# Optimization experiments

Measured on AMD Instinct MI355X. Metric: run time of the kernel, lower is better.

The kernel has to match this reference:

```python
import jax, jax.numpy as jnp
import numpy as np

LAMBDA = 0.5
ALPHA_PRE = 1.0
ALPHA_DA = 1.0

B, N, C, T, O = 8, 1024, 64, 12, 64


def setup_inputs() -> dict:
    key = jax.random.key(0)
    ks = jax.random.split(key, 10)
    s = 0.1  # keep tanh out of deep saturation, like xavier-init scales
    return {
        "x": jax.random.normal(ks[0], (B, N, C, T), dtype=jnp.float32),
        "static_adj": jax.random.uniform(ks[1], (N, N), dtype=jnp.float32) / N,
        "W0": jax.random.normal(ks[2], (C, O), dtype=jnp.float32) * s,
        "b0": jax.random.normal(ks[3], (O,), dtype=jnp.float32) * s,
        "Ws": jax.random.normal(ks[4], (T, C, O), dtype=jnp.float32) * s,
        "bs": jax.random.normal(ks[5], (T, O), dtype=jnp.float32) * s,
        "Wd": jax.random.normal(ks[6], (T, C, O), dtype=jnp.float32) * s,
        "bd": jax.random.normal(ks[7], (T, O), dtype=jnp.float32) * s,
        "E1": jax.random.normal(ks[8], (T, N, O), dtype=jnp.float32) * s,
        "E2": jax.random.normal(ks[9], (T, N, O), dtype=jnp.float32) * s,
    }


def reference(x, static_adj, W0, b0, Ws, bs, Wd, bd, E1, E2):
    # x: [B,N,C,T] -> [T,B,N,C] so the per-timestep layers vectorize over leading T.
    xt = jnp.transpose(x, (3, 0, 1, 2))  # [T,B,N,C]
    n = xt.shape[2]

    # shared top-level linear
    x0 = jnp.einsum('tbnc,co->tbno', xt, W0) + b0  # [T,B,N,O]

    # static GCN per timestep: linear(static_adj @ x_t)
    sagg = jnp.einsum('nm,tbmc->tbnc', static_adj, xt)
    static_out = jnp.einsum('tbnc,tco->tbno', sagg, Ws) + bs[:, None, None, :]

    # dynamic GCN: base = linear_t(x_t)
    base = jnp.einsum('tbnc,tco->tbno', xt, Wd) + bd[:, None, None, :]
    DE1 = jnp.tanh(ALPHA_PRE * (base * E1[:, None]))  # [T,B,N,O]
    DE2 = jnp.tanh(ALPHA_PRE * (base * E2[:, None]))
    # cross = DE1@DE2^T - DE2@DE1^T = M - M^T
    M = jnp.einsum('tbno,tbmo->tbnm', DE1, DE2)  # [T,B,N,N]
    DA = jax.nn.relu(jnp.tanh(ALPHA_DA * (M - jnp.swapaxes(M, -1, -2))))

    # symmetric degree normalization of (DA + I)
    DA = DA + jnp.eye(n, dtype=DA.dtype)
    rowsum = jnp.clip(DA.sum(axis=-1), 1e-12, None)
    d_inv_sqrt = rowsum ** -0.5
    DA = DA * d_inv_sqrt[..., :, None] * d_inv_sqrt[..., None, :]

    dagg = jnp.einsum('tbnm,tbmc->tbnc', DA, xt)
    dyn_out = jnp.einsum('tbnc,tco->tbno', dagg, Wd) + bd[:, None, None, :]

    fused = (LAMBDA - 0.025) * static_out + (1.0 - LAMBDA - 0.025) * dyn_out + 0.05 * x0
    return jnp.transpose(fused, (1, 2, 3, 0))  # [B,N,O,T]
```

## Files before the change

kernel.cpp:

```cpp
#include <hip/hip_runtime.h>

#define BB 8
#define NN 1024
#define CC 64
#define TT 12
#define OO 64

typedef unsigned short u16;
typedef __attribute__((ext_vector_type(8))) short s16x8;
typedef __attribute__((ext_vector_type(4))) float f32x4;
typedef __attribute__((ext_vector_type(4))) unsigned int u32x4;
typedef __attribute__((ext_vector_type(2))) unsigned int u32x2;

__device__ __forceinline__ u16 f2bu(float f){
  union { float f; unsigned u; } v; v.f = f;
  unsigned r = v.u + 0x7FFFu + ((v.u >> 16) & 1u);
  return (u16)(r >> 16);
}
__device__ __forceinline__ float b2f(u16 h){
  union { unsigned u; float f; } v; v.u = ((unsigned)h) << 16; return v.f;
}
__device__ __forceinline__ float relu_tanh(float d){
  float e = __expf(2.0f * d);
  return fmaxf(1.0f - 2.0f * __builtin_amdgcn_rcpf(e + 1.0f), 0.0f);
}
__device__ __forceinline__ float tanh_fast(float d){
  float e = __expf(2.0f * d);
  return 1.0f - 2.0f * __builtin_amdgcn_rcpf(e + 1.0f);
}
__device__ __forceinline__ float tanh_sgn(float x){
  float ax = fabsf(x);
  float e = __expf(2.0f * ax);
  float t = 1.0f - 2.0f * __builtin_amdgcn_rcpf(e + 1.0f);
  return x < 0.0f ? -t : t;
}

#define MFMA16(a,b,c) __builtin_amdgcn_mfma_f32_16x16x32_bf16((a),(b),(c),0,0,0)

__device__ __forceinline__ s16x8 ld72(const u16* s, int row0, int ko, int lane){
  return *(const s16x8*)(s + (row0 + (lane & 15)) * 72 + ko + ((lane >> 4) << 3));
}

__global__ __launch_bounds__(256) void k0_transpose(const float* __restrict__ x,
                                                    u16* __restrict__ xt){
  const int n = blockIdx.x, b = blockIdx.y;
  __shared__ float s[CC*TT];
  const float* src = x + (size_t)(b*NN + n)*CC*TT;
  for (int k = threadIdx.x; k < CC*TT; k += 256) s[k] = src[k];
  __syncthreads();
  for (int k = threadIdx.x; k < CC*TT; k += 256){
    const int t = k >> 6, c = k & 63;
    xt[(((size_t)t*BB + b)*NN + n)*CC + c] = f2bu(s[c*TT + t]);
  }
}

__global__ __launch_bounds__(256) void kprep(const float* __restrict__ adj,
                                             u16* __restrict__ adjb,
                                             float* __restrict__ rs){
  const size_t i = ((size_t)blockIdx.x*256 + threadIdx.x)*4;
  if (i < (size_t)NN*NN){
    const float4 v = *(const float4*)(adj + i);
    u16 o0=f2bu(v.x), o1=f2bu(v.y), o2=f2bu(v.z), o3=f2bu(v.w);
    adjb[i]=o0; adjb[i+1]=o1; adjb[i+2]=o2; adjb[i+3]=o3;
  }
  const size_t j = (size_t)blockIdx.x*256 + threadIdx.x;
  if (j < (size_t)TT*BB*NN) rs[j] = 1.0f;
}

__global__ __launch_bounds__(256) void k1_de(const u16* __restrict__ xt,
    const float* __restrict__ Wd, const float* __restrict__ bd,
    const float* __restrict__ E1, const float* __restrict__ E2,
    u16* __restrict__ DE1g, u16* __restrict__ DE2g){
  __shared__ __align__(16) u16 sWd[64*72];
  const int tid = threadIdx.x, lane = tid & 63, wid = tid >> 6;
  const int l15 = lane & 15, lr4 = lane >> 4;
  const int it = blockIdx.x, b = blockIdx.y, t = blockIdx.z;
  const int n0 = it * 64;
  for (int k = tid; k < 4096; k += 256){
    const int o = k & 63, c = k >> 6;
    sWd[o*72 + c] = f2bu(Wd[(size_t)t*4096 + c*64 + o]);
  }
  __syncthreads();
  const size_t tb = (size_t)t*BB + b;
  const u16* gx = xt + (tb*NN + n0)*CC;
  const int wrow = wid * 16;
  const f32x4 fz = {0.f,0.f,0.f,0.f};
  f32x4 acc[4] = {fz, fz, fz, fz};
  #pragma unroll
  for (int ks = 0; ks < 2; ++ks){
    const int ko = ks*32;
    const s16x8 a = *(const s16x8*)(gx + (wrow + l15)*CC + ko + (lr4 << 3));
    #pragma unroll
    for (int v = 0; v < 4; ++v)
      acc[v] = MFMA16(a, ld72(sWd, v*16, ko, lane), acc[v]);
  }
  #pragma unroll
  for (int v = 0; v < 4; ++v){
    const int o = v*16 + l15;
    const float bdv = bd[t*OO + o];
    #pragma unroll
    for (int e = 0; e < 4; ++e){
      const int n = n0 + wrow + (lr4 << 2) + e;
      const float base = acc[v][e] + bdv;
      const size_t eo = ((size_t)t*NN + n)*OO + o;
      const size_t so = (tb*NN + n)*OO + o;
      DE1g[so] = f2bu(tanh_sgn(base * E1[eo]));
      DE2g[so] = f2bu(tanh_sgn(base * E2[eo]));
    }
  }
}

__global__ __launch_bounds__(256) void k2a(const u16* __restrict__ DE1g,
    const u16* __restrict__ DE2g, float* __restrict__ rowsum){
  __shared__ __align__(16) u16 sb0[64*72], sb1[64*72];
  __shared__ __align__(16) u16 sb2[64*72], sb3[64*72];
  const int tid = threadIdx.x, lane = tid & 63, wid = tid >> 6;
  const int l15 = lane & 15, lr4 = lane >> 4;
  const int nwg = 8*BB*TT;
  const int logical = ((int)blockIdx.x & 7)*(nwg >> 3) + ((int)blockIdx.x >> 3);
  const int p = logical & 7;
  const size_t tb = (size_t)(logical >> 3);
  const int tiA = p, tiB = 15 - p;
  const u16* g1 = DE1g + tb*NN*OO;
  const u16* g2 = DE2g + tb*NN*OO;
  for (int k = tid; k < 512; k += 256){
    const int r = k >> 3, c = (k & 7) << 3;
    *(s16x8*)(sb0 + r*72 + c) = *(const s16x8*)(g1 + (size_t)(tiA*64 + r)*OO + c);
    s16x8 vA = *(const s16x8*)(g2 + (size_t)(tiA*64 + r)*OO + c);
    u32x4 wA = *(u32x4*)&vA; wA ^= 0x80008000u;
    *(u32x4*)(sb1 + r*72 + c) = wA;
    *(s16x8*)(sb2 + r*72 + c) = *(const s16x8*)(g1 + (size_t)(tiB*64 + r)*OO + c);
    s16x8 vB = *(const s16x8*)(g2 + (size_t)(tiB*64 + r)*OO + c);
    u32x4 wB = *(u32x4*)&vB; wB ^= 0x80008000u;
    *(u32x4*)(sb3 + r*72 + c) = wB;
  }
  __syncthreads();
  const int wrow = wid * 16;
  s16x8 a1A[2], na2A[2], a1B[2], na2B[2];
  #pragma unroll
  for (int ks = 0; ks < 2; ++ks){
    a1A[ks]  = ld72(sb0, wrow, ks*32, lane);
    na2A[ks] = ld72(sb1, wrow, ks*32, lane);
    a1B[ks]  = ld72(sb2, wrow, ks*32, lane);
    na2B[ks] = ld72(sb3, wrow, ks*32, lane);
  }
  const int srow = tid >> 2, sc0 = (tid & 3) << 4;
  s16x8 pB1a,pB1b, pB2a,pB2b;
#define LOADT(TJ) do { \
    pB1a = *(const s16x8*)(g2 + (size_t)((TJ)*64 + srow)*OO + sc0); \
    pB1b = *(const s16x8*)(g2 + (size_t)((TJ)*64 + srow)*OO + sc0 + 8); \
    pB2a = *(const s16x8*)(g1 + (size_t)((TJ)*64 + srow)*OO + sc0); \
    pB2b = *(const s16x8*)(g1 + (size_t)((TJ)*64 + srow)*OO + sc0 + 8); \
  } while (0)
  LOADT(p);
  float rpA[4] = {0.f,0.f,0.f,0.f}, rpB[4] = {0.f,0.f,0.f,0.f};
  const f32x4 fz = {0.f,0.f,0.f,0.f};
  float* rsg = rowsum + tb*NN;
  __syncthreads();
  for (int tj = p; tj < 16; ++tj){
    u16* sJ1 = ((tj - p) & 1) ? sb2 : sb0;
    u16* sJ2 = ((tj - p) & 1) ? sb3 : sb1;
    *(s16x8*)(sJ1 + srow*72 + sc0)     = pB1a;
    *(s16x8*)(sJ1 + srow*72 + sc0 + 8) = pB1b;
    *(s16x8*)(sJ2 + srow*72 + sc0)     = pB2a;
    *(s16x8*)(sJ2 + srow*72 + sc0 + 8) = pB2b;
    __syncthreads();
    if (tj < 15) LOADT(tj + 1);
    s16x8 b1[4], b2[4], b1h[4], b2h[4];
    #pragma unroll
    for (int v = 0; v < 4; ++v){
      b1[v]  = ld72(sJ1, v*16, 0,  lane);
      b2[v]  = ld72(sJ2, v*16, 0,  lane);
      b1h[v] = ld72(sJ1, v*16, 32, lane);
      b2h[v] = ld72(sJ2, v*16, 32, lane);
    }
    {
      f32x4 z[4];
      #pragma unroll
      for (int v = 0; v < 4; ++v){
        z[v] = MFMA16(a1A[0],  b1[v],  fz);
        z[v] = MFMA16(na2A[0], b2[v],  z[v]);
        z[v] = MFMA16(a1A[1],  b1h[v], z[v]);
        z[v] = MFMA16(na2A[1], b2h[v], z[v]);
      }
      float colp[4] = {0.f,0.f,0.f,0.f};
      #pragma unroll
      for (int v = 0; v < 4; ++v)
        #pragma unroll
        for (int e = 0; e < 4; ++e){
          const float th = tanh_fast(z[v][e]);
          rpA[e]  += fmaxf(th, 0.f);
          colp[v] += fmaxf(-th, 0.f);
        }
      if (tj > tiA){
        #pragma unroll
        for (int v = 0; v < 4; ++v){
          float c = colp[v];
          c += __shfl_xor(c, 16); c += __shfl_xor(c, 32);
          if (lane < 16) atomicAdd(&rsg[tj*64 + v*16 + lane], c);
        }
      }
    }
    if (tj >= tiB){
      f32x4 z[4];
      #pragma unroll
      for (int v = 0; v < 4; ++v){
        z[v] = MFMA16(a1B[0],  b1[v],  fz);
        z[v] = MFMA16(na2B[0], b2[v],  z[v]);
        z[v] = MFMA16(a1B[1],  b1h[v], z[v]);
        z[v] = MFMA16(na2B[1], b2h[v], z[v]);
      }
      float colp[4] = {0.f,0.f,0.f,0.f};
      #pragma unroll
      for (int v = 0; v < 4; ++v)
        #pragma unroll
        for (int e = 0; e < 4; ++e){
          const float th = tanh_fast(z[v][e]);
          rpB[e]  += fmaxf(th, 0.f);
          colp[v] += fmaxf(-th, 0.f);
        }
      if (tj > tiB){
        #pragma unroll
        for (int v = 0; v < 4; ++v){
          float c = colp[v];
          c += __shfl_xor(c, 16); c += __shfl_xor(c, 32);
          if (lane < 16) atomicAdd(&rsg[tj*64 + v*16 + lane], c);
        }
      }
    }
  }
#undef LOADT
  #pragma unroll
  for (int e = 0; e < 4; ++e){
    float r = rpA[e];
    r += __shfl_xor(r, 1); r += __shfl_xor(r, 2);
    r += __shfl_xor(r, 4); r += __shfl_xor(r, 8);
    if (l15 == 0) atomicAdd(&rsg[tiA*64 + wrow + (lr4 << 2) + e], r);
  }
  #pragma unroll
  for (int e = 0; e < 4; ++e){
    float r = rpB[e];
    r += __shfl_xor(r, 1); r += __shfl_xor(r, 2);
    r += __shfl_xor(r, 4); r += __shfl_xor(r, 8);
    if (l15 == 0) atomicAdd(&rsg[tiB*64 + wrow + (lr4 << 2) + e], r);
  }
}

__global__ __launch_bounds__(256) void k3b(const u16* __restrict__ xt,
    const float* __restrict__ Wd, const float* __restrict__ Ws,
    const float* __restrict__ W0, const float* __restrict__ bd,
    const float* __restrict__ bs, const float* __restrict__ b0,
    const float* __restrict__ rowsum, u16* __restrict__ xdvT,
    u16* __restrict__ xswT, u16* __restrict__ x0w){
  __shared__ __align__(16) u16 sW[64*72];
  const int tid = threadIdx.x, lane = tid & 63, wid = tid >> 6;
  const int l15 = lane & 15, lr4 = lane >> 4;
  const int it = blockIdx.x, b = blockIdx.y, t = blockIdx.z;
  const size_t tb = (size_t)t*BB + b;
  const int n0 = it * 128, wrow = wid * 32;
  const float* dvb = rowsum + tb*NN + n0;
  float dis[2][4];
  #pragma unroll
  for (int u = 0; u < 2; ++u)
    #pragma unroll
    for (int e = 0; e < 4; ++e)
      dis[u][e] = rsqrtf(dvb[wrow + u*16 + (lr4 << 2) + e]);
  float badd[4];
  #pragma unroll
  for (int v = 0; v < 4; ++v){
    const int o = v*16 + l15;
    badd[v] = 0.475f*(bd[t*OO + o] + bs[t*OO + o]) + 0.05f*b0[o];
  }
  const u16* gx = xt + (tb*NN + n0)*CC;
  const f32x4 fz = {0.f,0.f,0.f,0.f};
  for (int pass = 0; pass < 3; ++pass){
    __syncthreads();
    {
      const float* Wsrc = (pass == 0) ? (Wd + (size_t)t*4096)
                        : (pass == 1) ? (Ws + (size_t)t*4096) : W0;
      const float scale = (pass == 2) ? 0.05f : 0.475f;
      for (int k = tid; k < 4096; k += 256){
        const int o = k & 63, c = k >> 6;
        sW[o*72 + c] = f2bu(scale * Wsrc[c*64 + o]);
      }
    }
    __syncthreads();
    f32x4 acc[2][4];
    #pragma unroll
    for (int u = 0; u < 2; ++u)
      #pragma unroll
      for (int v = 0; v < 4; ++v) acc[u][v] = fz;
    #pragma unroll
    for (int ks = 0; ks < 2; ++ks){
      const int ko = ks*32;
      s16x8 bw[4];
      #pragma unroll
      for (int v = 0; v < 4; ++v) bw[v] = ld72(sW, v*16, ko, lane);
      #pragma unroll
      for (int u = 0; u < 2; ++u){
        const s16x8 a = *(const s16x8*)(gx + (wrow + u*16 + l15)*CC + ko + (lr4 << 3));
        #pragma unroll
        for (int v = 0; v < 4; ++v) acc[u][v] = MFMA16(a, bw[v], acc[u][v]);
      }
    }
    #pragma unroll
    for (int u = 0; u < 2; ++u)
      #pragma unroll
      for (int v = 0; v < 4; ++v){
        const int o = v*16 + l15;
        #pragma unroll
        for (int e = 0; e < 4; ++e){
          const int nl = wrow + u*16 + (lr4 << 2) + e;
          float val = acc[u][v][e];
          if (pass == 0)      xdvT[(tb*OO + o)*NN + n0 + nl] = f2bu(val * dis[u][e]);
          else if (pass == 1) xswT[(tb*OO + o)*NN + n0 + nl] = f2bu(val);
          else                x0w[(tb*NN + n0 + nl)*OO + o]  = f2bu(val + badd[v]);
        }
      }
  }
}

__global__ __launch_bounds__(256) void k4s(const u16* __restrict__ adjb,
    const u16* __restrict__ xswT, u16* __restrict__ outSta){
  __shared__ __align__(16) u16 sJ[64*72], sS[64*72];
  const int tid = threadIdx.x, lane = tid & 63, wid = tid >> 6;
  const int l15 = lane & 15, lr4 = lane >> 4;
  const int nwg = 16*BB*TT;
  const int logical = ((int)blockIdx.x & 7)*(nwg >> 3) + ((int)blockIdx.x >> 3);
  const int ti = logical / (BB*TT);
  const size_t tb = (size_t)(logical % (BB*TT));
  const u16* xs = xswT + tb*OO*NN;
  const int i0 = ti * 64, wrow = wid * 16;
  const int srow = tid >> 2, sc0 = (tid & 3) << 4;
  s16x8 pJa, pJb, pSa, pSb;
#define LOADS(TJ) do { \
    pJa = *(const s16x8*)(adjb + (size_t)(i0 + srow)*NN + (TJ)*64 + sc0); \
    pJb = *(const s16x8*)(adjb + (size_t)(i0 + srow)*NN + (TJ)*64 + sc0 + 8); \
    pSa = *(const s16x8*)(xs   + (size_t)srow*NN + (TJ)*64 + sc0); \
    pSb = *(const s16x8*)(xs   + (size_t)srow*NN + (TJ)*64 + sc0 + 8); \
  } while (0)
  LOADS(0);
  const f32x4 fz = {0.f,0.f,0.f,0.f};
  f32x4 as_[4] = {fz,fz,fz,fz};
  for (int tj = 0; tj < 16; ++tj){
    *(s16x8*)(sJ + srow*72 + sc0)     = pJa;
    *(s16x8*)(sJ + srow*72 + sc0 + 8) = pJb;
    *(s16x8*)(sS + srow*72 + sc0)     = pSa;
    *(s16x8*)(sS + srow*72 + sc0 + 8) = pSb;
    __syncthreads();
    if (tj < 15) LOADS(tj + 1);
    const s16x8 aJ0 = ld72(sJ, wrow, 0,  lane);
    const s16x8 aJ1 = ld72(sJ, wrow, 32, lane);
    #pragma unroll
    for (int v = 0; v < 4; ++v){
      as_[v] = MFMA16(aJ0, ld72(sS, v*16, 0,  lane), as_[v]);
      as_[v] = MFMA16(aJ1, ld72(sS, v*16, 32, lane), as_[v]);
    }
    __syncthreads();
  }
#undef LOADS
  #pragma unroll
  for (int v = 0; v < 4; ++v){
    const int o = v*16 + l15;
    #pragma unroll
    for (int e = 0; e < 4; ++e){
      const int n = i0 + wrow + (lr4 << 2) + e;
      outSta[(tb*NN + n)*OO + o] = f2bu(as_[v][e]);
    }
  }
}

__global__ __launch_bounds__(256) void k2bf(const u16* __restrict__ DE1g,
    const u16* __restrict__ DE2g, const u16* __restrict__ xdvT,
    const float* __restrict__ rowsum, float* __restrict__ outT){
  __shared__ __align__(16) u16 sB1[64*72], sB2[64*72], sXD[64*72];
  const int tid = threadIdx.x, lane = tid & 63, wid = tid >> 6;
  const int l15 = lane & 15, lr4 = lane >> 4;
  const int nwg = 16*BB*TT;
  const int logical = ((int)blockIdx.x & 7)*(nwg >> 3) + ((int)blockIdx.x >> 3);
  const int ti = logical & 15;
  const size_t tb = (size_t)(logical >> 4);
  const u16* g1 = DE1g + tb*NN*OO;
  const u16* g2 = DE2g + tb*NN*OO;
  const u16* xd = xdvT + tb*OO*NN;
  const float* dv = rowsum + tb*NN;
  const int i0 = ti * 64;
  for (int k = tid; k < 512; k += 256){
    const int r = k >> 3, c = (k & 7) << 3;
    *(s16x8*)(sB1 + r*72 + c) = *(const s16x8*)(g1 + (size_t)(i0 + r)*OO + c);
    s16x8 v = *(const s16x8*)(g2 + (size_t)(i0 + r)*OO + c);
    u32x4 w = *(u32x4*)&v; w ^= 0x80008000u;
    *(u32x4*)(sB2 + r*72 + c) = w;
  }
  __syncthreads();
  const int wrow = wid * 16;
  s16x8 a1[2], na2[2];
  #pragma unroll
  for (int ks = 0; ks < 2; ++ks){
    a1[ks]  = ld72(sB1, wrow, ks*32, lane);
    na2[ks] = ld72(sB2, wrow, ks*32, lane);
  }
  const int srow = tid >> 2, sc0 = (tid & 3) << 4;
  const int g0 = sc0 >> 2;
  int kap[4];
  #pragma unroll
  for (int q = 0; q < 4; ++q){
    const int g = g0 + q;
    kap[q] = ((g & 3) << 3) + (((g >> 2) & 1) << 2) + ((g >> 3) << 5);
  }
  s16x8 pB1a,pB1b, pB2a,pB2b, pXDa,pXDb;
#define LOADT(TJ) do { \
    pB1a = *(const s16x8*)(g2 + (size_t)((TJ)*64 + srow)*OO + sc0); \
    pB1b = *(const s16x8*)(g2 + (size_t)((TJ)*64 + srow)*OO + sc0 + 8); \
    pB2a = *(const s16x8*)(g1 + (size_t)((TJ)*64 + srow)*OO + sc0); \
    pB2b = *(const s16x8*)(g1 + (size_t)((TJ)*64 + srow)*OO + sc0 + 8); \
    pXDa = *(const s16x8*)(xd + (size_t)srow*NN + (TJ)*64 + sc0); \
    pXDb = *(const s16x8*)(xd + (size_t)srow*NN + (TJ)*64 + sc0 + 8); \
  } while (0)
  LOADT(0);
  const f32x4 fz = {0.f,0.f,0.f,0.f};
  f32x4 ad[4] = {fz,fz,fz,fz};
  __syncthreads();
  for (int tj = 0; tj < 16; ++tj){
    *(s16x8*)(sB1 + srow*72 + sc0)     = pB1a;
    *(s16x8*)(sB1 + srow*72 + sc0 + 8) = pB1b;
    *(s16x8*)(sB2 + srow*72 + sc0)     = pB2a;
    *(s16x8*)(sB2 + srow*72 + sc0 + 8) = pB2b;
    {
      const u32x4 xa = *(const u32x4*)&pXDa;
      const u32x4 xb = *(const u32x4*)&pXDb;
      u32x2 h;
      h[0] = xa[0]; h[1] = xa[1];
      *(u32x2*)(sXD + srow*72 + kap[0]) = h;
      h[0] = xa[2]; h[1] = xa[3];
      *(u32x2*)(sXD + srow*72 + kap[1]) = h;
      h[0] = xb[0]; h[1] = xb[1];
      *(u32x2*)(sXD + srow*72 + kap[2]) = h;
      h[0] = xb[2]; h[1] = xb[3];
      *(u32x2*)(sXD + srow*72 + kap[3]) = h;
    }
    __syncthreads();
    if (tj < 15) LOADT(tj + 1);
    f32x4 y[4];
    #pragma unroll
    for (int v = 0; v < 4; ++v){
      y[v] = MFMA16(ld72(sB1, v*16, 0,  lane), a1[0],  fz);
      y[v] = MFMA16(ld72(sB2, v*16, 0,  lane), na2[0], y[v]);
      y[v] = MFMA16(ld72(sB1, v*16, 32, lane), a1[1],  y[v]);
      y[v] = MFMA16(ld72(sB2, v*16, 32, lane), na2[1], y[v]);
    }
    float q[4][4];
    #pragma unroll
    for (int v = 0; v < 4; ++v)
      #pragma unroll
      for (int e = 0; e < 4; ++e)
        q[v][e] = relu_tanh(y[v][e]);
    u32x4 w0, w1;
    asm("v_cvt_pk_bf16_f32 %0, %1, %2" : "=v"(w0[0]) : "v"(q[0][0]), "v"(q[0][1]));
    asm("v_cvt_pk_bf16_f32 %0, %1, %2" : "=v"(w0[1]) : "v"(q[0][2]), "v"(q[0][3]));
    asm("v_cvt_pk_bf16_f32 %0, %1, %2" : "=v"(w0[2]) : "v"(q[1][0]), "v"(q[1][1]));
    asm("v_cvt_pk_bf16_f32 %0, %1, %2" : "=v"(w0[3]) : "v"(q[1][2]), "v"(q[1][3]));
    asm("v_cvt_pk_bf16_f32 %0, %1, %2" : "=v"(w1[0]) : "v"(q[2][0]), "v"(q[2][1]));
    asm("v_cvt_pk_bf16_f32 %0, %1, %2" : "=v"(w1[1]) : "v"(q[2][2]), "v"(q[2][3]));
    asm("v_cvt_pk_bf16_f32 %0, %1, %2" : "=v"(w1[2]) : "v"(q[3][0]), "v"(q[3][1]));
    asm("v_cvt_pk_bf16_f32 %0, %1, %2" : "=v"(w1[3]) : "v"(q[3][2]), "v"(q[3][3]));
    const s16x8 pa0 = *(const s16x8*)&w0;
    const s16x8 pa1 = *(const s16x8*)&w1;
    #pragma unroll
    for (int v = 0; v < 4; ++v){
      ad[v] = MFMA16(pa0, ld72(sXD, v*16, 0,  lane), ad[v]);
      ad[v] = MFMA16(pa1, ld72(sXD, v*16, 32, lane), ad[v]);
    }
    __syncthreads();
  }
#undef LOADT
  const int grow0 = i0 + wrow + (lr4 << 2);
  float disv[4];
  #pragma unroll
  for (int e = 0; e < 4; ++e) disv[e] = rsqrtf(dv[grow0 + e]);
  #pragma unroll
  for (int v = 0; v < 4; ++v){
    const int o = v*16 + l15;
    #pragma unroll
    for (int e = 0; e < 4; ++e){
      const float xw = b2f(xd[(size_t)o*NN + grow0 + e]);
      outT[(tb*NN + grow0 + e)*OO + o] = disv[e]*(ad[v][e] + xw);
    }
  }
}

__global__ __launch_bounds__(256) void k5(const float* __restrict__ outT,
                                          const u16* __restrict__ x0w,
                                          const u16* __restrict__ outSta,
                                          float* __restrict__ out){
  __shared__ float s[16*64*12];
  const int tid = threadIdx.x;
  const int nb = blockIdx.x, b = blockIdx.y;
  const int n0 = nb * 16;
  for (int t = 0; t < TT; ++t){
    for (int k = tid; k < 1024; k += 256){
      const int r = k >> 6, o = k & 63;
      const size_t idx = (((size_t)t*BB + b)*NN + n0 + r)*OO + o;
      s[(r*64 + o)*12 + t] = outT[idx] + b2f(x0w[idx]) + b2f(outSta[idx]);
    }
  }
  __syncthreads();
  float* dst = out + (size_t)(b*NN + n0)*OO*TT;
  for (int k = tid; k < 16*64*12; k += 256) dst[k] = s[k];
}

extern "C" void kernel_launch(void* const* d_in, const int* in_sizes, int n_in,
                              void* d_out, int out_size, void* d_ws, size_t ws_size,
                              hipStream_t stream) {
  const float* x   = (const float*)d_in[0];
  const float* adj = (const float*)d_in[1];
  const float* W0  = (const float*)d_in[2];
  const float* b0  = (const float*)d_in[3];
  const float* Ws  = (const float*)d_in[4];
  const float* bs  = (const float*)d_in[5];
  const float* Wd  = (const float*)d_in[6];
  const float* bd  = (const float*)d_in[7];
  const float* E1  = (const float*)d_in[8];
  const float* E2  = (const float*)d_in[9];
  float* out = (float*)d_out;

  char* w = (char*)d_ws;
  size_t off = 0;
  auto take = [&](size_t bytes) -> char* {
    char* p = w + off;
    off += bytes; off = (off + 255) & ~(size_t)255;
    return p;
  };
  const size_t NE = (size_t)TT*BB*NN*OO;
  u16*   xt    = (u16*)  take(NE*2);
  u16*   adjb  = (u16*)  take((size_t)NN*NN*2);
  u16*   DE1   = (u16*)  take(NE*2);
  u16*   DE2   = (u16*)  take(NE*2);
  float* rowsum= (float*)take((size_t)TT*BB*NN*4);
  u16*   xdvT  = (u16*)  take(NE*2);
  u16*   xswT  = (u16*)  take(NE*2);
  u16*   x0w   = (u16*)  take(NE*2);
  u16*   outSta= (u16*)  take(NE*2);
  float* outT  = (float*)take(NE*4);

  k0_transpose<<<dim3(NN, BB), 256, 0, stream>>>(x, xt);
  kprep<<<dim3((NN*NN)/1024), 256, 0, stream>>>(adj, adjb, rowsum);
  k1_de<<<dim3(16, BB, TT), 256, 0, stream>>>(xt, Wd, bd, E1, E2, DE1, DE2);
  k2a<<<dim3(8*BB*TT), 256, 0, stream>>>(DE1, DE2, rowsum);
  k3b<<<dim3(8, BB, TT), 256, 0, stream>>>(xt, Wd, Ws, W0, bd, bs, b0,
                                           rowsum, xdvT, xswT, x0w);
  k4s<<<dim3(16*BB*TT), 256, 0, stream>>>(adjb, xswT, outSta);
  k2bf<<<dim3(16*BB*TT), 256, 0, stream>>>(DE1, DE2, xdvT, rowsum, outT);
  k5<<<dim3(NN/16, BB), 256, 0, stream>>>(outT, x0w, outSta, out);
}
```

Baseline: 217.3 us.

## Double-buffer LDS tiles and load k2bf DE operands directly into registers

Both GEMM kernels now double-buffer their LDS tiles, which removes the trailing barrier in each tile iteration. In k2bf, the DE2/DE1 B-operand fragments for the M-tile are loaded from global memory straight into MFMA register layout. This skips the LDS staging of those fragments and removes two shared arrays, leaving only the xd tile in LDS. The cost is more VGPRs (16 extra s16x8 fragments), which may lower occupancy, plus less coalesced global loads that rely on L2 reuse.

```diff
diff --git a/kernel.cpp b/kernel.cpp
--- a/kernel.cpp
+++ b/kernel.cpp
@@ -322,7 +322,7 @@
 
 __global__ __launch_bounds__(256) void k4s(const u16* __restrict__ adjb,
     const u16* __restrict__ xswT, u16* __restrict__ outSta){
-  __shared__ __align__(16) u16 sJ[64*72], sS[64*72];
+  __shared__ __align__(16) u16 sJ[2][64*72], sS[2][64*72];
   const int tid = threadIdx.x, lane = tid & 63, wid = tid >> 6;
   const int l15 = lane & 15, lr4 = lane >> 4;
   const int nwg = 16*BB*TT;
@@ -343,20 +343,20 @@
   const f32x4 fz = {0.f,0.f,0.f,0.f};
   f32x4 as_[4] = {fz,fz,fz,fz};
   for (int tj = 0; tj < 16; ++tj){
-    *(s16x8*)(sJ + srow*72 + sc0)     = pJa;
-    *(s16x8*)(sJ + srow*72 + sc0 + 8) = pJb;
-    *(s16x8*)(sS + srow*72 + sc0)     = pSa;
-    *(s16x8*)(sS + srow*72 + sc0 + 8) = pSb;
+    const int cur = tj & 1;
+    *(s16x8*)(sJ[cur] + srow*72 + sc0)     = pJa;
+    *(s16x8*)(sJ[cur] + srow*72 + sc0 + 8) = pJb;
+    *(s16x8*)(sS[cur] + srow*72 + sc0)     = pSa;
+    *(s16x8*)(sS[cur] + srow*72 + sc0 + 8) = pSb;
     __syncthreads();
     if (tj < 15) LOADS(tj + 1);
-    const s16x8 aJ0 = ld72(sJ, wrow, 0,  lane);
-    const s16x8 aJ1 = ld72(sJ, wrow, 32, lane);
+    const s16x8 aJ0 = ld72(sJ[cur], wrow, 0,  lane);
+    const s16x8 aJ1 = ld72(sJ[cur], wrow, 32, lane);
     #pragma unroll
     for (int v = 0; v < 4; ++v){
-      as_[v] = MFMA16(aJ0, ld72(sS, v*16, 0,  lane), as_[v]);
-      as_[v] = MFMA16(aJ1, ld72(sS, v*16, 32, lane), as_[v]);
-    }
-    __syncthreads();
+      as_[v] = MFMA16(aJ0, ld72(sS[cur], v*16, 0,  lane), as_[v]);
+      as_[v] = MFMA16(aJ1, ld72(sS[cur], v*16, 32, lane), as_[v]);
+    }
   }
 #undef LOADS
   #pragma unroll
@@ -373,7 +373,7 @@
 __global__ __launch_bounds__(256) void k2bf(const u16* __restrict__ DE1g,
     const u16* __restrict__ DE2g, const u16* __restrict__ xdvT,
     const float* __restrict__ rowsum, float* __restrict__ outT){
-  __shared__ __align__(16) u16 sB1[64*72], sB2[64*72], sXD[64*72];
+  __shared__ __align__(16) u16 sXD[2][64*72];
   const int tid = threadIdx.x, lane = tid & 63, wid = tid >> 6;
   const int l15 = lane & 15, lr4 = lane >> 4;
   const int nwg = 16*BB*TT;
@@ -387,18 +387,18 @@
   const int i0 = ti * 64;
   for (int k = tid; k < 512; k += 256){
     const int r = k >> 3, c = (k & 7) << 3;
-    *(s16x8*)(sB1 + r*72 + c) = *(const s16x8*)(g1 + (size_t)(i0 + r)*OO + c);
+    *(s16x8*)(sXD[0] + r*72 + c) = *(const s16x8*)(g1 + (size_t)(i0 + r)*OO + c);
     s16x8 v = *(const s16x8*)(g2 + (size_t)(i0 + r)*OO + c);
     u32x4 w = *(u32x4*)&v; w ^= 0x80008000u;
-    *(u32x4*)(sB2 + r*72 + c) = w;
+    *(u32x4*)(sXD[1] + r*72 + c) = w;
   }
   __syncthreads();
   const int wrow = wid * 16;
   s16x8 a1[2], na2[2];
   #pragma unroll
   for (int ks = 0; ks < 2; ++ks){
-    a1[ks]  = ld72(sB1, wrow, ks*32, lane);
-    na2[ks] = ld72(sB2, wrow, ks*32, lane);
+    a1[ks]  = ld72(sXD[0], wrow, ks*32, lane);
+    na2[ks] = ld72(sXD[1], wrow, ks*32, lane);
   }
   const int srow = tid >> 2, sc0 = (tid & 3) << 4;
   const int g0 = sc0 >> 2;
@@ -408,47 +408,49 @@
     const int g = g0 + q;
     kap[q] = ((g & 3) << 3) + (((g >> 2) & 1) << 2) + ((g >> 3) << 5);
   }
-  s16x8 pB1a,pB1b, pB2a,pB2b, pXDa,pXDb;
-#define LOADT(TJ) do { \
-    pB1a = *(const s16x8*)(g2 + (size_t)((TJ)*64 + srow)*OO + sc0); \
-    pB1b = *(const s16x8*)(g2 + (size_t)((TJ)*64 + srow)*OO + sc0 + 8); \
-    pB2a = *(const s16x8*)(g1 + (size_t)((TJ)*64 + srow)*OO + sc0); \
-    pB2b = *(const s16x8*)(g1 + (size_t)((TJ)*64 + srow)*OO + sc0 + 8); \
+  s16x8 jb1[8], jb2[8];
+  s16x8 pXDa, pXDb;
+#define PREFJ(TJ) do { \
+    _Pragma("unroll") for (int ks = 0; ks < 2; ++ks) \
+    _Pragma("unroll") for (int v = 0; v < 4; ++v){ \
+      const int go = ((TJ)*64 + v*16 + l15)*OO + ks*32 + (lr4 << 3); \
+      jb1[ks*4+v] = *(const s16x8*)(g2 + go); \
+      jb2[ks*4+v] = *(const s16x8*)(g1 + go); \
+    } } while (0)
+#define LOADXD(TJ) do { \
     pXDa = *(const s16x8*)(xd + (size_t)srow*NN + (TJ)*64 + sc0); \
     pXDb = *(const s16x8*)(xd + (size_t)srow*NN + (TJ)*64 + sc0 + 8); \
   } while (0)
-  LOADT(0);
+  PREFJ(0);
+  LOADXD(0);
   const f32x4 fz = {0.f,0.f,0.f,0.f};
   f32x4 ad[4] = {fz,fz,fz,fz};
   __syncthreads();
   for (int tj = 0; tj < 16; ++tj){
-    *(s16x8*)(sB1 + srow*72 + sc0)     = pB1a;
-    *(s16x8*)(sB1 + srow*72 + sc0 + 8) = pB1b;
-    *(s16x8*)(sB2 + srow*72 + sc0)     = pB2a;
-    *(s16x8*)(sB2 + srow*72 + sc0 + 8) = pB2b;
+    const int cur = tj & 1;
     {
       const u32x4 xa = *(const u32x4*)&pXDa;
       const u32x4 xb = *(const u32x4*)&pXDb;
       u32x2 h;
       h[0] = xa[0]; h[1] = xa[1];
-      *(u32x2*)(sXD + srow*72 + kap[0]) = h;
+      *(u32x2*)(sXD[cur] + srow*72 + kap[0]) = h;
       h[0] = xa[2]; h[1] = xa[3];
-      *(u32x2*)(sXD + srow*72 + kap[1]) = h;
+      *(u32x2*)(sXD[cur] + srow*72 + kap[1]) = h;
       h[0] = xb[0]; h[1] = xb[1];
-      *(u32x2*)(sXD + srow*72 + kap[2]) = h;
+      *(u32x2*)(sXD[cur] + srow*72 + kap[2]) = h;
       h[0] = xb[2]; h[1] = xb[3];
-      *(u32x2*)(sXD + srow*72 + kap[3]) = h;
+      *(u32x2*)(sXD[cur] + srow*72 + kap[3]) = h;
     }
     __syncthreads();
-    if (tj < 15) LOADT(tj + 1);
     f32x4 y[4];
     #pragma unroll
     for (int v = 0; v < 4; ++v){
-      y[v] = MFMA16(ld72(sB1, v*16, 0,  lane), a1[0],  fz);
-      y[v] = MFMA16(ld72(sB2, v*16, 0,  lane), na2[0], y[v]);
-      y[v] = MFMA16(ld72(sB1, v*16, 32, lane), a1[1],  y[v]);
-      y[v] = MFMA16(ld72(sB2, v*16, 32, lane), na2[1], y[v]);
-    }
+      y[v] = MFMA16(jb1[v],   a1[0],  fz);
+      y[v] = MFMA16(jb2[v],   na2[0], y[v]);
+      y[v] = MFMA16(jb1[4+v], a1[1],  y[v]);
+      y[v] = MFMA16(jb2[4+v], na2[1], y[v]);
+    }
+    if (tj < 15){ PREFJ(tj + 1); LOADXD(tj + 1); }
     float q[4][4];
     #pragma unroll
     for (int v = 0; v < 4; ++v)
@@ -468,12 +470,12 @@
     const s16x8 pa1 = *(const s16x8*)&w1;
     #pragma unroll
     for (int v = 0; v < 4; ++v){
-      ad[v] = MFMA16(pa0, ld72(sXD, v*16, 0,  lane), ad[v]);
-      ad[v] = MFMA16(pa1, ld72(sXD, v*16, 32, lane), ad[v]);
-    }
-    __syncthreads();
-  }
-#undef LOADT
+      ad[v] = MFMA16(pa0, ld72(sXD[cur], v*16, 0,  lane), ad[v]);
+      ad[v] = MFMA16(pa1, ld72(sXD[cur], v*16, 32, lane), ad[v]);
+    }
+  }
+#undef PREFJ
+#undef LOADXD
   const int grow0 = i0 + wrow + (lr4 << 2);
   float disv[4];
   #pragma unroll
```

Result: slower. 338.5 us (+55.8%).
